# Optimization experiments

Hardware: AMD Instinct MI355X
Metric: run time of the kernel (lower is better)

The kernel has to match this reference:

```python
import jax, jax.numpy as jnp
import numpy as np

T, B = 110, 256            # max_seq_len, num dialogues (all length T)
N = T * B                  # total graph nodes
DM = 300                   # fused input dim (100 text + 100 audio + 100 visual)
F = 200                    # 2*D_e node feature dim
H = 64                     # graph_hidden_size
R = 8                      # num relations (2 speakers x 2 speakers x 2 directions)
NB = 30                    # RGCN num_bases
NC = 7                     # n_classes
DA = F + H                 # matchatt / classifier input dim
WP, WF = 10, 10            # window_past, window_future

def _build_edges():
    src, dst = [], []
    for j in range(T):
        for i in range(max(0, j - WP), min(T, j + WF + 1)):
            src.append(j); dst.append(i)
    return np.asarray(src, np.int32), np.asarray(dst, np.int32)

SRC_T, DST_T = _build_edges()                    # per-dialogue edge endpoints [E0]
DIRN = (SRC_T >= DST_T).astype(np.int32)         # direction bit: '0' iff j < i
OFF = np.arange(B, dtype=np.int32) * T
SRC = (OFF[:, None] + SRC_T[None, :]).reshape(-1)  # global src node ids, dialogue-major
DST = (OFF[:, None] + DST_T[None, :]).reshape(-1)
E = SRC.shape[0]

def _p(key, shape, scale=0.05):
    return (jax.random.normal(key, shape) * scale).astype(jnp.float32)

def setup_inputs():
    key = jax.random.key(0)
    ks = jax.random.split(key, 16)
    return {
        "textf": jax.random.normal(ks[0], (T, B, 100), jnp.float32),
        "acouf": jax.random.normal(ks[1], (T, B, 100), jnp.float32),
        "visuf": jax.random.normal(ks[2], (T, B, 100), jnp.float32),
        "speakers": jax.random.randint(ks[3], (T, B), 0, 2, jnp.int32),
        "Wf": _p(ks[4], (DM, F)), "bf": jnp.zeros((F,), jnp.float32),
        "basis": _p(ks[5], (NB, F, H)), "comp": _p(ks[6], (R, NB)),
        "root": _p(ks[7], (F, H)), "b_rgcn": jnp.zeros((H,), jnp.float32),
        "Wrel": _p(ks[8], (H, H)), "brel": jnp.zeros((H,), jnp.float32),
        "Wroot2": _p(ks[9], (H, H)),
        "Wma": _p(ks[10], (DA, DA)), "bma": jnp.zeros((DA,), jnp.float32),
        "Wl": _p(ks[11], (DA, H)), "bl": jnp.zeros((H,), jnp.float32),
        "Ws": _p(ks[12], (H, NC)), "bs": jnp.zeros((NC,), jnp.float32),
    }

def reference(textf, acouf, visuf, speakers, Wf, bf, basis, comp, root, b_rgcn,
              Wrel, brel, Wroot2, Wma, bma, Wl, bl, Ws, bs):
    src, dst = jnp.asarray(SRC), jnp.asarray(DST)
    # feature fusion: concat modalities -> linear, [T,B,300] -> [T,B,200]
    feats = jnp.concatenate([textf, acouf, visuf], axis=-1) @ Wf + bf
    x = jnp.transpose(feats, (1, 0, 2)).reshape(N, F)       # node features, dialogue-major
    # edge types from speaker ids: key '{s0}{s1}{dir}' -> s0*4 + s1*2 + dir
    s0 = speakers[SRC_T]                                    # [E0, B]
    s1 = speakers[DST_T]
    et = (s0 * 4 + s1 * 2 + jnp.asarray(DIRN)[:, None]).T.reshape(-1)  # [E]
    # --- RGCNConv (basis decomposition, per-relation mean aggregation) ---
    Wrels = jnp.einsum('rb,bfh->rfh', comp, basis)          # [R,F,H]
    xr = jnp.einsum('nf,rfh->nrh', x, Wrels)                # [N,R,H] projected per relation
    msg = xr[src, et]                                       # [E,H] gather
    seg = dst * R + et
    summ = jax.ops.segment_sum(msg, seg, num_segments=N * R).reshape(N, R, H)
    cnt = jax.ops.segment_sum(jnp.ones((E,), jnp.float32), seg, num_segments=N * R).reshape(N, R, 1)
    h1 = (summ / jnp.maximum(cnt, 1.0)).sum(1) + x @ root + b_rgcn   # [N,H]
    # --- GraphConv (sum aggregation) ---
    agg = jax.ops.segment_sum(h1[src], dst, num_segments=N)
    h2 = agg @ Wrel + brel + h1 @ Wroot2                    # [N,H]
    emotions = jnp.concatenate([x, h2], axis=-1)            # [N,DA]
    # --- nodal MatchingAttention ('general2') over full equal-length dialogues ---
    M = emotions.reshape(B, T, DA).transpose(1, 0, 2)       # [T,B,DA]
    umask = jnp.ones((B, T), jnp.float32)
    Xq = M @ Wma + bma                                      # [T,B,DA] transformed queries
    scores = jnp.einsum('tbd,sbd->tbs', Xq, M * umask.T[:, :, None])
    scores = jnp.tanh(scores * umask[None])
    alpha = jax.nn.softmax(scores, axis=-1) * umask[None]
    alpha = alpha / alpha.sum(-1, keepdims=True)
    att = jnp.einsum('tbs,sbd->tbd', alpha, M)              # [T,B,DA]
    hidden = jax.nn.relu(att @ Wl + bl)                     # dropout = identity (eval)
    logits = hidden @ Ws + bs
    logp = jax.nn.log_softmax(logits, axis=-1)              # [T,B,NC]
    # unpad/concat per dialogue (all lengths == T) -> [B*T, NC]
    return jnp.transpose(logp, (1, 0, 2)).reshape(N, NC)
```

## Files before the change

kernel.cpp:

```cpp
#include <hip/hip_runtime.h>

#define TT   110
#define BBD  256
#define NND  28160
#define WIN  10

typedef __bf16 bf16x8 __attribute__((ext_vector_type(8)));
typedef __bf16 bf16x4 __attribute__((ext_vector_type(4)));
typedef float  f32x4  __attribute__((ext_vector_type(4)));

__device__ __forceinline__ int imax(int a, int b){ return a > b ? a : b; }
__device__ __forceinline__ int imin(int a, int b){ return a < b ? a : b; }


__global__ __launch_bounds__(256) void wrels_k(
    const float* __restrict__ basis, const float* __restrict__ comp,
    const float* __restrict__ root, float* __restrict__ wrels)
{
  int idx = blockIdx.x * 256 + threadIdx.x;
  if (idx >= 115200) return;
  int r = idx / 12800, fh = idx % 12800;
  float v;
  if (r < 8) {
    v = 0.f;
    #pragma unroll
    for (int nb = 0; nb < 30; ++nb) v += comp[r*30 + nb] * basis[nb*12800 + fh];
  } else {
    v = root[fh];
  }
  wrels[idx] = v;
}

__global__ __launch_bounds__(256) void prep_k(
    const float* __restrict__ textf, const float* __restrict__ acouf,
    const float* __restrict__ visuf, const float* __restrict__ wrels,
    const float* __restrict__ Wf, const float* __restrict__ Wma,
    const float* __restrict__ Wl, const float* __restrict__ Wrel,
    const float* __restrict__ Wroot2, __bf16* __restrict__ Ain,
    __bf16* __restrict__ img)
{
  constexpr int T0 = 1126400;
  constexpr int T1 = T0 + 10240;
  constexpr int T2 = T1 + 18432;
  constexpr int T3 = T2 + 12800;
  constexpr int T4 = T3 + 2560;
  constexpr int T5 = T4 + 1024;
  for (int c = blockIdx.x * 256 + threadIdx.x; c < T5; c += gridDim.x * 256) {
    bf16x8 v;
    __bf16* dst;
    if (c < T0) {
      const int m = c / 40, cc = c - m * 40;
      const int col0 = cc << 3;
      const size_t ab = (size_t)m * 100;
      #pragma unroll
      for (int e = 0; e < 8; ++e) {
        const int col = col0 + e;
        float x = (col < 100) ? textf[ab + col]
                : (col < 200) ? acouf[ab + col - 100]
                : (col < 300) ? visuf[ab + col - 200] : 0.f;
        v[e] = (__bf16)x;
      }
      dst = Ain + (size_t)m * 320 + col0;
    } else if (c < T1) {
      const int r = c - T0;
      const int cb = r / 2560, r2 = r - cb * 2560;
      const int col = r2 / 40, ch = r2 - col * 40;
      const int cs = (ch & ~7) | ((ch ^ col) & 7);
      const int gc = (cb << 6) + col;
      #pragma unroll
      for (int e = 0; e < 8; ++e) {
        const int k = (cs << 3) + e;
        v[e] = (__bf16)((k < 300 && gc < 200) ? Wf[k*200 + gc] : 0.f);
      }
      dst = img + cb * 20480 + col * 320 + (ch << 3);
    } else if (c < T2) {
      const int r = c - T1;
      const int cb = r / 2048, r2 = r - cb * 2048;
      const int col = r2 / 32, ch = r2 - col * 32;
      const int cs = (ch & ~7) | ((ch ^ col) & 7);
      #pragma unroll
      for (int e = 0; e < 8; ++e) {
        const int k = (cs << 3) + e;
        v[e] = (__bf16)((k < 200) ? wrels[cb*12800 + k*64 + col] : 0.f);
      }
      dst = img + 81920 + cb * 16384 + col * 256 + (ch << 3);
    } else if (c < T3) {
      const int r = c - T2;
      const int cb = r / 2560, r2 = r - cb * 2560;
      const int col = r2 / 40, ch = r2 - col * 40;
      const int cs = (ch & ~7) | ((ch ^ col) & 7);
      const int gc = (cb << 6) + col;
      #pragma unroll
      for (int e = 0; e < 8; ++e) {
        const int k = (cs << 3) + e;
        v[e] = (__bf16)((k < 264 && gc < 264) ? Wma[k*264 + gc] : 0.f);
      }
      dst = img + 229376 + cb * 20480 + col * 320 + (ch << 3);
    } else if (c < T4) {
      const int r = c - T3;
      const int col = r / 40, ch = r - col * 40;
      const int cs = (ch & ~7) | ((ch ^ col) & 7);
      #pragma unroll
      for (int e = 0; e < 8; ++e) {
        const int k = (cs << 3) + e;
        v[e] = (__bf16)((k < 264) ? Wl[k*64 + col] : 0.f);
      }
      dst = img + 331776 + col * 320 + (ch << 3);
    } else {
      const int r = c - T4;
      const int col = r / 16, ch = r - col * 16;
      const int cs = (ch & ~7) | ((ch ^ col) & 7);
      #pragma unroll
      for (int e = 0; e < 8; ++e) {
        const int k = (cs << 3) + e;
        v[e] = (__bf16)((k < 64) ? Wrel[k*64 + col] : Wroot2[(k-64)*64 + col]);
      }
      dst = img + 352256 + col * 128 + (ch << 3);
    }
    *(bf16x8*)dst = v;
  }
}

template<int MODE, int NK, int KSP, int NCB, int OUT>
__global__ __launch_bounds__(256) void bgemm_k(
    const __bf16* __restrict__ A0, const __bf16* __restrict__ A1,
    const __bf16* __restrict__ Bimg, const float* __restrict__ bias,
    void* __restrict__ Cv, int Ncols)
{
  __shared__ __align__(16) __bf16 Bsh[64][KSP];
  const int tid = threadIdx.x;
  constexpr int NWT = 440 * NCB;
  constexpr int q = NWT >> 3;
  const int bid = blockIdx.x;
  const int w = (bid & 7) * q + (bid >> 3);
  const int m0 = (w / NCB) << 6;
  const int cb = w % NCB;
  const int n0 = cb << 6;

  {
    const bf16x8* src = (const bf16x8*)(Bimg + (size_t)cb * (64 * KSP));
    bf16x8* dst = (bf16x8*)&Bsh[0][0];
    constexpr int NIT = (64 * KSP / 8) / 256;
    #pragma unroll
    for (int c = 0; c < NIT; ++c) dst[c * 256 + tid] = src[c * 256 + tid];
  }
  __syncthreads();

  const int wid = tid >> 6, lane = tid & 63;
  const int wm = wid >> 1, wn = wid & 1;
  const int fr = lane & 15;
  const int fk = (lane >> 4) << 3;
  const int row0 = (lane >> 4) << 2;

  f32x4 acc[2][2];
  #pragma unroll
  for (int f = 0; f < 2; ++f)
    #pragma unroll
    for (int g = 0; g < 2; ++g) acc[f][g] = (f32x4){0.f,0.f,0.f,0.f};

  #pragma unroll
  for (int kt = 0; kt < NK; ++kt) {
    const int ko = (kt << 5) + fk;
    bf16x8 af[2];
    #pragma unroll
    for (int f = 0; f < 2; ++f) {
      const int ra = m0 + wm*32 + f*16 + fr;
      if constexpr (MODE == 2) {
        af[f] = (ko < 200) ? *(const bf16x8*)(A0 + (size_t)ra*200 + ko)
                           : *(const bf16x8*)(A1 + (size_t)ra*64 + (ko - 200));
      } else {
        constexpr int SA = (MODE == 0) ? 320 : 200;
        af[f] = *(const bf16x8*)(A0 + (size_t)ra*SA + ko);
      }
    }
    bf16x8 bfv[2];
    #pragma unroll
    for (int g = 0; g < 2; ++g) {
      const int rb_ = wn*32 + g*16 + fr;
      bfv[g] = *(const bf16x8*)&Bsh[rb_][(((ko >> 3) ^ (rb_ & 7)) << 3)];
    }
    #pragma unroll
    for (int f = 0; f < 2; ++f)
      #pragma unroll
      for (int g = 0; g < 2; ++g)
        acc[f][g] = __builtin_amdgcn_mfma_f32_16x16x32_bf16(af[f], bfv[g], acc[f][g], 0, 0, 0);
  }

  #pragma unroll
  for (int g = 0; g < 2; ++g) {
    const int col = n0 + wn*32 + g*16 + fr;
    if (col < Ncols) {
      const float bv = bias ? bias[col] : 0.f;
      #pragma unroll
      for (int f = 0; f < 2; ++f) {
        const int gm0 = m0 + wm*32 + f*16 + row0;
        #pragma unroll
        for (int r2 = 0; r2 < 4; ++r2) {
          const float v = acc[f][g][r2] + bv;
          const int gm = gm0 + r2;
          if constexpr (OUT == 1) {
            ((__bf16*)Cv)[(size_t)gm * Ncols + col] = (__bf16)v;
          } else {
            __bf16* Cb = (__bf16*)Cv;
            const size_t o = (size_t)gm * 288 + col;
            const __bf16 hi = (__bf16)v;
            Cb[o] = hi;
            Cb[(size_t)288 * NND + o] = (__bf16)(v - (float)hi);
          }
        }
      }
    }
  }
}

__global__ __launch_bounds__(512) void dialog_k(
    const __bf16* __restrict__ xr, const int* __restrict__ spk,
    const float* __restrict__ brg, const __bf16* __restrict__ Wgcimg,
    const float* __restrict__ brel, __bf16* __restrict__ h2)
{
  __shared__ __align__(16) __bf16 Xsh[75][320];
  __shared__ float  h1f[65][68];
  __shared__ __align__(16) __bf16 aggbf[56][72];
  __shared__ int ssp[TT];
  __shared__ int pc[TT + 1];
  const int bid = blockIdx.x;
  const int b = bid >> 1, half = bid & 1;
  const int t0   = half ? 55 : 0;
  const int H1LO = half ? 45 : 0;
  const int XLO  = half ? 35 : 0;
  const int tid = threadIdx.x;
  if (tid < TT) ssp[tid] = spk[tid * BBD + b];
  __syncthreads();
  if (tid < 64) {
    int v = (tid < TT) ? ssp[tid] : 0;
    #pragma unroll
    for (int o = 1; o < 64; o <<= 1) { const int u = __shfl_up(v, o); if (tid >= o) v += u; }
    pc[tid + 1] = v;
    const int tot = __shfl(v, 63);
    int v2 = (tid + 64 < TT) ? ssp[tid + 64] : 0;
    #pragma unroll
    for (int o = 1; o < 64; o <<= 1) { const int u = __shfl_up(v2, o); if (tid >= o) v2 += u; }
    if (tid + 64 < TT) pc[tid + 65] = tot + v2;
    if (tid == 0) pc[0] = 0;
  }
  for (int i = tid << 3; i < 75 * 320; i += 512 << 3) {
    const int xl = i / 320, off = i - xl * 320;
    const int j = XLO + xl;
    const size_t base = ((size_t)j * BBD + b) * 576;
    const int col = (off < 256) ? ((ssp[j] << 8) + off) : (256 + off);
    *(bf16x8*)&Xsh[xl][off] = *(const bf16x8*)&xr[base + col];
  }
  __syncthreads();
  const int w8 = tid >> 6, lane = tid & 63;
  const float bias = brg[lane];
  for (int lh = w8; lh < 65; lh += 8) {
    const int t = H1LO + lh;
    const int si2 = ssp[t] << 1;
    const int jlo = imax(t - WIN, 0), jhi = imin(t + WIN, TT - 1);
    const int n1d0 = pc[t] - pc[jlo];
    const int n0d0 = (t - jlo) - n1d0;
    const int n1d1 = pc[jhi + 1] - pc[t];
    const int n0d1 = (jhi - t + 1) - n1d1;
    const float r00 = 1.f / (float)imax(n0d0, 1);
    const float r10 = 1.f / (float)imax(n1d0, 1);
    const float r01 = 1.f / (float)imax(n0d1, 1);
    const float r11 = 1.f / (float)imax(n1d1, 1);
    float a = 0.f;
    if (t >= WIN && t < TT - WIN) {
      #pragma unroll
      for (int dj = -WIN; dj <= WIN; ++dj) {
        const int j = t + dj;
        const float v = (float)Xsh[j - XLO][((si2 + ((dj >= 0) ? 1 : 0)) << 6) + lane];
        const float w = (dj >= 0) ? (ssp[j] ? r11 : r01) : (ssp[j] ? r10 : r00);
        a = fmaf(w, v, a);
      }
    } else {
      #pragma unroll
      for (int dj = -WIN; dj <= WIN; ++dj) {
        const int j = t + dj;
        const int jc = imin(imax(j, XLO), XLO + 74);
        const float v = (float)Xsh[jc - XLO][((si2 + ((dj >= 0) ? 1 : 0)) << 6) + lane];
        float w = (dj >= 0) ? (ssp[jc] ? r11 : r01) : (ssp[jc] ? r10 : r00);
        if (j < 0 || j >= TT) w = 0.f;
        a = fmaf(w, v, a);
      }
    }
    a += (float)Xsh[t - XLO][256 + lane] + bias;
    h1f[lh][lane] = a;
  }
  __syncthreads();
  for (int lt = w8; lt < 55; lt += 8) {
    const int t = t0 + lt;
    float a = 0.f;
    if (t >= WIN && t < TT - WIN) {
      #pragma unroll
      for (int dj = -WIN; dj <= WIN; ++dj)
        a += h1f[t + dj - H1LO][lane];
    } else {
      #pragma unroll
      for (int dj = -WIN; dj <= WIN; ++dj) {
        const int j = t + dj;
        const int jc = imin(imax(j, H1LO), H1LO + 64);
        const float m = ((j >= 0) && (j < TT)) ? 1.f : 0.f;
        a = fmaf(m, h1f[jc - H1LO][lane], a);
      }
    }
    aggbf[lt][lane] = (__bf16)a;
  }
  __syncthreads();
  if (w8 < 4) {
    const int wm = w8 >> 1, wn = w8 & 1;
    const int fr = lane & 15, fk = (lane >> 4) << 3, row0 = (lane >> 4) << 2;
    const int lhh = t0 - H1LO;
    f32x4 acc[2][2];
    #pragma unroll
    for (int f = 0; f < 2; ++f)
      #pragma unroll
      for (int g = 0; g < 2; ++g) acc[f][g] = (f32x4){0.f,0.f,0.f,0.f};
    #pragma unroll
    for (int kt = 0; kt < 4; ++kt) {
      const int ko = (kt << 5) + fk;
      bf16x8 af[2];
      #pragma unroll
      for (int f = 0; f < 2; ++f) {
        const int tr = wm*32 + f*16 + fr;
        if (tr < 55) {
          if (ko < 64) {
            af[f] = *(const bf16x8*)&aggbf[tr][ko];
          } else {
            const float* src = &h1f[tr + lhh][ko - 64];
            const float4 u0 = ((const float4*)src)[0];
            const float4 u1 = ((const float4*)src)[1];
            af[f] = (bf16x8){(__bf16)u0.x,(__bf16)u0.y,(__bf16)u0.z,(__bf16)u0.w,
                             (__bf16)u1.x,(__bf16)u1.y,(__bf16)u1.z,(__bf16)u1.w};
          }
        } else af[f] = (bf16x8){0,0,0,0,0,0,0,0};
      }
      bf16x8 bfv[2];
      #pragma unroll
      for (int g = 0; g < 2; ++g) {
        const int rb_ = wn*32 + g*16 + fr;
        bfv[g] = *(const bf16x8*)(Wgcimg + rb_*128 + (((ko >> 3) ^ (rb_ & 7)) << 3));
      }
      #pragma unroll
      for (int f = 0; f < 2; ++f)
        #pragma unroll
        for (int g = 0; g < 2; ++g)
          acc[f][g] = __builtin_amdgcn_mfma_f32_16x16x32_bf16(af[f], bfv[g], acc[f][g], 0, 0, 0);
    }
    #pragma unroll
    for (int g = 0; g < 2; ++g) {
      const int col = wn*32 + g*16 + fr;
      const float bv = brel[col];
      #pragma unroll
      for (int f = 0; f < 2; ++f) {
        const int tr0 = wm*32 + f*16 + row0;
        #pragma unroll
        for (int r2 = 0; r2 < 4; ++r2) {
          const int tr = tr0 + r2;
          if (tr < 55) {
            const int t = t0 + tr;
            h2[((size_t)t * BBD + b) * 64 + col] = (__bf16)(acc[f][g][r2] + bv);
          }
        }
      }
    }
  }
}

__global__ __launch_bounds__(448) void attn_mfma_k(
    const __bf16* __restrict__ x, const __bf16* __restrict__ h2,
    const __bf16* __restrict__ Xq, __bf16* __restrict__ att)
{
  __shared__ __align__(16) __bf16 Msh [TT ][272];
  __shared__ __align__(16) __bf16 MTsh[264][136];
  __shared__ __align__(16) __bf16 Ash [112][136];
  const int b = blockIdx.x;
  const int tid = threadIdx.x;

  for (int idx = tid; idx < TT * 66; idx += 448) {
    const int s = idx / 66, c4 = idx % 66;
    const size_t node = (size_t)s * BBD + b;
    bf16x4 pk;
    if (c4 < 50) pk = *(const bf16x4*)&x [node * 200 + (c4 << 2)];
    else         pk = *(const bf16x4*)&h2[node * 64 + ((c4 - 50) << 2)];
    *(bf16x4*)&Msh[s][c4 << 2] = pk;
    const int d = c4 << 2;
    MTsh[d+0][s] = pk[0]; MTsh[d+1][s] = pk[1];
    MTsh[d+2][s] = pk[2]; MTsh[d+3][s] = pk[3];
  }
  for (int idx = tid; idx < 264 * 26; idx += 448) MTsh[idx / 26][110 + idx % 26] = (__bf16)0.f;
  for (int idx = tid; idx < 112 * 24; idx += 448) Ash[idx / 24][112 + idx % 24] = (__bf16)0.f;
  __syncthreads();

  const int wid = tid >> 6, lane = tid & 63;
  const int t0 = wid << 4;
  const int fr = lane & 15;
  const int g  = lane >> 4;
  const int fk = g << 3;

  f32x4 sacc[7];
  #pragma unroll
  for (int st = 0; st < 7; ++st) sacc[st] = (f32x4){0.f,0.f,0.f,0.f};
  const int trow = t0 + fr;
  const size_t arow = ((size_t)(trow < TT ? trow : TT - 1) * BBD + b) * 288;
  const __bf16* XqLo = Xq + (size_t)288 * NND;
  for (int kst = 0; kst < 9; ++kst) {
    const int k0 = kst << 5;
    bf16x8 aqh = *(const bf16x8*)&Xq  [arow + k0 + fk];
    bf16x8 aql = *(const bf16x8*)&XqLo[arow + k0 + fk];
    if (kst == 8 && fk != 0) {
      aqh = (bf16x8){0,0,0,0,0,0,0,0};
      aql = (bf16x8){0,0,0,0,0,0,0,0};
    }
    #pragma unroll
    for (int st = 0; st < 7; ++st) {
      bf16x8 bq;
      if (kst < 8) bq = *(const bf16x8*)&Msh[st*16 + fr][k0 + fk];
      else bq = (fk == 0) ? *(const bf16x8*)&Msh[st*16 + fr][256]
                          : (bf16x8){0,0,0,0,0,0,0,0};
      sacc[st] = __builtin_amdgcn_mfma_f32_16x16x32_bf16(aqh, bq, sacc[st], 0, 0, 0);
      sacc[st] = __builtin_amdgcn_mfma_f32_16x16x32_bf16(aql, bq, sacc[st], 0, 0, 0);
    }
  }

  #pragma unroll
  for (int r = 0; r < 4; ++r) {
    float tv[7];
    #pragma unroll
    for (int st = 0; st < 7; ++st) {
      const float e2 = __expf(2.f * sacc[st][r]);
      tv[st] = 1.f - 2.f / (e2 + 1.f);
    }
    if (fr >= 14) tv[6] = -3.0e38f;
    float mx = fmaxf(fmaxf(fmaxf(tv[0],tv[1]), fmaxf(tv[2],tv[3])),
                     fmaxf(fmaxf(tv[4],tv[5]), tv[6]));
    #pragma unroll
    for (int o = 8; o >= 1; o >>= 1) mx = fmaxf(mx, __shfl_xor(mx, o, 16));
    float e[7], sum = 0.f;
    #pragma unroll
    for (int st = 0; st < 7; ++st) { e[st] = __expf(tv[st] - mx); sum += e[st]; }
    #pragma unroll
    for (int o = 8; o >= 1; o >>= 1) sum += __shfl_xor(sum, o, 16);
    const float inv = 1.f / sum;
    const int tr = t0 + (g << 2) + r;
    #pragma unroll
    for (int st = 0; st < 7; ++st) Ash[tr][st*16 + fr] = (__bf16)(e[st] * inv);
  }
  __syncthreads();

  const int tr2 = t0 + (g << 2);
  for (int dt = 0; dt < 17; ++dt) {
    const int d0 = dt << 4;
    f32x4 pacc = (f32x4){0.f,0.f,0.f,0.f};
    #pragma unroll
    for (int kst = 0; kst < 4; ++kst) {
      const int k0 = kst << 5;
      const bf16x8 pa = *(const bf16x8*)&Ash [t0 + fr][k0 + fk];
      const bf16x8 pb = *(const bf16x8*)&MTsh[d0 + fr][k0 + fk];
      pacc = __builtin_amdgcn_mfma_f32_16x16x32_bf16(pa, pb, pacc, 0, 0, 0);
    }
    const int col = d0 + fr;
    if (col < 264) {
      #pragma unroll
      for (int r = 0; r < 4; ++r) {
        const int t = tr2 + r;
        if (t < TT) att[((size_t)t * BBD + b) * 264 + col] = (__bf16)pacc[r];
      }
    }
  }
}

__global__ __launch_bounds__(256) void final_k(
    const __bf16* __restrict__ att, const __bf16* __restrict__ Wlimg,
    const float* __restrict__ bl, const float* __restrict__ Wsm,
    const float* __restrict__ bsm, float* __restrict__ out)
{
  constexpr int KSP = 320;
  __shared__ __align__(16) __bf16 Bsh[64][KSP];
  __shared__ float hidf[64][68];
  __shared__ float Wssh[64][8];
  const int tid = threadIdx.x;
  const int bid = blockIdx.x;
  const int m0 = ((bid & 7) * 55 + (bid >> 3)) << 6;
  {
    const bf16x8* src = (const bf16x8*)Wlimg;
    bf16x8* dst = (bf16x8*)&Bsh[0][0];
    #pragma unroll
    for (int c = 0; c < 10; ++c) dst[c * 256 + tid] = src[c * 256 + tid];
    for (int i = tid; i < 512; i += 256) {
      const int k = i >> 3, cc = i & 7;
      Wssh[k][cc] = (cc < 7) ? Wsm[k*7 + cc] : 0.f;
    }
  }
  __syncthreads();
  const int wid = tid >> 6, lane = tid & 63;
  const int wm = wid >> 1, wn = wid & 1;
  const int fr = lane & 15, fk = (lane >> 4) << 3, row0 = (lane >> 4) << 2;
  f32x4 acc[2][2];
  #pragma unroll
  for (int f = 0; f < 2; ++f)
    #pragma unroll
    for (int g = 0; g < 2; ++g) acc[f][g] = (f32x4){0.f,0.f,0.f,0.f};
  #pragma unroll
  for (int kt = 0; kt < 9; ++kt) {
    const int ko = (kt << 5) + fk;
    bf16x8 af[2];
    #pragma unroll
    for (int f = 0; f < 2; ++f) {
      const int ra = m0 + wm*32 + f*16 + fr;
      af[f] = (ko < 264) ? *(const bf16x8*)(att + (size_t)ra*264 + ko)
                         : (bf16x8){0,0,0,0,0,0,0,0};
    }
    bf16x8 bfv[2];
    #pragma unroll
    for (int g = 0; g < 2; ++g) {
      const int rb_ = wn*32 + g*16 + fr;
      bfv[g] = *(const bf16x8*)&Bsh[rb_][(((ko >> 3) ^ (rb_ & 7)) << 3)];
    }
    #pragma unroll
    for (int f = 0; f < 2; ++f)
      #pragma unroll
      for (int g = 0; g < 2; ++g)
        acc[f][g] = __builtin_amdgcn_mfma_f32_16x16x32_bf16(af[f], bfv[g], acc[f][g], 0, 0, 0);
  }
  #pragma unroll
  for (int g = 0; g < 2; ++g) {
    const int col = wn*32 + g*16 + fr;
    const float bv = bl[col];
    #pragma unroll
    for (int f = 0; f < 2; ++f) {
      const int lr0 = wm*32 + f*16 + row0;
      #pragma unroll
      for (int r2 = 0; r2 < 4; ++r2)
        hidf[lr0 + r2][col] = fmaxf(acc[f][g][r2] + bv, 0.f);
    }
  }
  __syncthreads();
  const int c = tid & 7;
  const float bc = (c < 7) ? bsm[c] : 0.f;
  #pragma unroll
  for (int p = 0; p < 2; ++p) {
    const int lr = (p << 5) + (tid >> 3);
    float lg = -3.0e38f;
    if (c < 7) {
      lg = bc;
      #pragma unroll
      for (int k = 0; k < 64; ++k) lg += hidf[lr][k] * Wssh[k][c];
    }
    float mx = lg;
    #pragma unroll
    for (int o = 4; o >= 1; o >>= 1) mx = fmaxf(mx, __shfl_xor(mx, o, 8));
    float e = (c < 7) ? __expf(lg - mx) : 0.f;
    float sm = e;
    #pragma unroll
    for (int o = 4; o >= 1; o >>= 1) sm += __shfl_xor(sm, o, 8);
    if (c < 7) {
      const int gm = m0 + lr;
      const int t = gm >> 8, bb = gm & 255;
      out[((size_t)bb * TT + t) * 7 + c] = lg - mx - __logf(sm);
    }
  }
}

extern "C" void kernel_launch(void* const* d_in, const int* in_sizes, int n_in,
                              void* d_out, int out_size, void* d_ws, size_t ws_size,
                              hipStream_t stream)
{
  const float* textf  = (const float*)d_in[0];
  const float* acouf  = (const float*)d_in[1];
  const float* visuf  = (const float*)d_in[2];
  const int*   spk    = (const int*)  d_in[3];
  const float* Wf     = (const float*)d_in[4];
  const float* bfv    = (const float*)d_in[5];
  const float* basis  = (const float*)d_in[6];
  const float* comp   = (const float*)d_in[7];
  const float* root   = (const float*)d_in[8];
  const float* brg    = (const float*)d_in[9];
  const float* Wrel   = (const float*)d_in[10];
  const float* brel   = (const float*)d_in[11];
  const float* Wroot2 = (const float*)d_in[12];
  const float* Wma    = (const float*)d_in[13];
  const float* bma    = (const float*)d_in[14];
  const float* Wl     = (const float*)d_in[15];
  const float* bl     = (const float*)d_in[16];
  const float* Wsm    = (const float*)d_in[17];
  const float* bsm    = (const float*)d_in[18];

  float* ws = (float*)d_ws;
  float*  wrels = ws;
  __bf16* img   = (__bf16*)(ws + 115200);
  __bf16* Ain   = (__bf16*)(ws + 295424);
  __bf16* xb    = (__bf16*)(ws + 4801024);
  __bf16* xr    = (__bf16*)(ws + 7617024);
  __bf16* h2    = (__bf16*)(ws + 15727104);
  __bf16* Xqb   = (__bf16*)(ws + 16628224);
  __bf16* attb  = xr;
  float*  outp  = (float*)d_out;

  __bf16* Wfimg  = img;
  __bf16* wrimg  = img + 81920;
  __bf16* Wmaimg = img + 229376;
  __bf16* Wlimg  = img + 331776;
  __bf16* Wgcimg = img + 352256;

  wrels_k<<<450, 256, 0, stream>>>(basis, comp, root, wrels);
  prep_k<<<2048, 256, 0, stream>>>(textf, acouf, visuf, wrels, Wf, Wma, Wl,
                                   Wrel, Wroot2, Ain, img);
  bgemm_k<0,10,320,4,1><<<1760, 256, 0, stream>>>(Ain, nullptr, Wfimg, bfv, xb, 200);
  bgemm_k<1,7,256,9,1><<<3960, 256, 0, stream>>>(xb, nullptr, wrimg, nullptr, xr, 576);
  dialog_k<<<512, 512, 0, stream>>>(xr, spk, brg, Wgcimg, brel, h2);
  bgemm_k<2,9,320,5,2><<<2200, 256, 0, stream>>>(xb, h2, Wmaimg, bma, Xqb, 264);
  attn_mfma_k<<<256, 448, 0, stream>>>(xb, h2, Xqb, attb);
  final_k<<<440, 256, 0, stream>>>(attb, Wlimg, bl, Wsm, bsm, outp);
}
```

Measured before the change: 153.7 us.

## Fuse final classifier into attention kernel and skip unused relation-GEMM stores

The final projection (Wl GEMM, ReLU, Ws logits, log-softmax) moves into the attention kernel. The attention output stays in shared memory (reusing Msh) instead of being written to global memory and read back by a separate launch. The relation GEMM epilogue also writes only the column blocks matching each source node's speaker (plus the root block), which cuts global store traffic. In exchange, the fused tail runs on only 256 blocks with Wl read straight from global memory, and it relies on downstream code reading only the speaker-matching columns.

```diff
diff --git a/kernel.cpp b/kernel.cpp
--- a/kernel.cpp
+++ b/kernel.cpp
@@ -125,7 +125,7 @@
 __global__ __launch_bounds__(256) void bgemm_k(
     const __bf16* __restrict__ A0, const __bf16* __restrict__ A1,
     const __bf16* __restrict__ Bimg, const float* __restrict__ bias,
-    void* __restrict__ Cv, int Ncols)
+    void* __restrict__ Cv, int Ncols, const int* __restrict__ spkm)
 {
   __shared__ __align__(16) __bf16 Bsh[64][KSP];
   const int tid = threadIdx.x;
@@ -187,25 +187,34 @@
   }
 
   #pragma unroll
-  for (int g = 0; g < 2; ++g) {
-    const int col = n0 + wn*32 + g*16 + fr;
-    if (col < Ncols) {
-      const float bv = bias ? bias[col] : 0.f;
-      #pragma unroll
-      for (int f = 0; f < 2; ++f) {
-        const int gm0 = m0 + wm*32 + f*16 + row0;
+  for (int f = 0; f < 2; ++f) {
+    const int gm0 = m0 + wm*32 + f*16 + row0;
+    int sp[4];
+    if constexpr (MODE == 1) {
+      #pragma unroll
+      for (int r2 = 0; r2 < 4; ++r2) sp[r2] = spkm[gm0 + r2];
+    }
+    #pragma unroll
+    for (int g = 0; g < 2; ++g) {
+      const int col = n0 + wn*32 + g*16 + fr;
+      if (col < Ncols) {
+        const float bv = bias ? bias[col] : 0.f;
         #pragma unroll
         for (int r2 = 0; r2 < 4; ++r2) {
           const float v = acc[f][g][r2] + bv;
           const int gm = gm0 + r2;
-          if constexpr (OUT == 1) {
-            ((__bf16*)Cv)[(size_t)gm * Ncols + col] = (__bf16)v;
-          } else {
-            __bf16* Cb = (__bf16*)Cv;
-            const size_t o = (size_t)gm * 288 + col;
-            const __bf16 hi = (__bf16)v;
-            Cb[o] = hi;
-            Cb[(size_t)288 * NND + o] = (__bf16)(v - (float)hi);
+          bool dow = true;
+          if constexpr (MODE == 1) dow = (cb == 8) || ((cb >> 2) == sp[r2]);
+          if (dow) {
+            if constexpr (OUT == 1) {
+              ((__bf16*)Cv)[(size_t)gm * Ncols + col] = (__bf16)v;
+            } else {
+              __bf16* Cb = (__bf16*)Cv;
+              const size_t o = (size_t)gm * 288 + col;
+              const __bf16 hi = (__bf16)v;
+              Cb[o] = hi;
+              Cb[(size_t)288 * NND + o] = (__bf16)(v - (float)hi);
+            }
           }
         }
       }
@@ -368,9 +377,11 @@
   }
 }
 
-__global__ __launch_bounds__(448) void attn_mfma_k(
+__global__ __launch_bounds__(448) void attn_fused_k(
     const __bf16* __restrict__ x, const __bf16* __restrict__ h2,
-    const __bf16* __restrict__ Xq, __bf16* __restrict__ att)
+    const __bf16* __restrict__ Xq, const __bf16* __restrict__ Wlimg,
+    const float* __restrict__ bl, const float* __restrict__ Wsm,
+    const float* __restrict__ bsm, float* __restrict__ out)
 {
   __shared__ __align__(16) __bf16 Msh [TT ][272];
   __shared__ __align__(16) __bf16 MTsh[264][136];
@@ -398,6 +409,7 @@
   const int fr = lane & 15;
   const int g  = lane >> 4;
   const int fk = g << 3;
+  const int row0 = g << 2;
 
   f32x4 sacc[7];
   #pragma unroll
@@ -449,6 +461,7 @@
   }
   __syncthreads();
 
+  __bf16 (*attsh)[272] = Msh;
   const int tr2 = t0 + (g << 2);
   for (int dt = 0; dt < 17; ++dt) {
     const int d0 = dt << 4;
@@ -465,100 +478,68 @@
       #pragma unroll
       for (int r = 0; r < 4; ++r) {
         const int t = tr2 + r;
-        if (t < TT) att[((size_t)t * BBD + b) * 264 + col] = (__bf16)pacc[r];
-      }
-    }
-  }
-}
-
-__global__ __launch_bounds__(256) void final_k(
-    const __bf16* __restrict__ att, const __bf16* __restrict__ Wlimg,
-    const float* __restrict__ bl, const float* __restrict__ Wsm,
-    const float* __restrict__ bsm, float* __restrict__ out)
-{
-  constexpr int KSP = 320;
-  __shared__ __align__(16) __bf16 Bsh[64][KSP];
-  __shared__ float hidf[64][68];
-  __shared__ float Wssh[64][8];
-  const int tid = threadIdx.x;
-  const int bid = blockIdx.x;
-  const int m0 = ((bid & 7) * 55 + (bid >> 3)) << 6;
-  {
-    const bf16x8* src = (const bf16x8*)Wlimg;
-    bf16x8* dst = (bf16x8*)&Bsh[0][0];
-    #pragma unroll
-    for (int c = 0; c < 10; ++c) dst[c * 256 + tid] = src[c * 256 + tid];
-    for (int i = tid; i < 512; i += 256) {
-      const int k = i >> 3, cc = i & 7;
-      Wssh[k][cc] = (cc < 7) ? Wsm[k*7 + cc] : 0.f;
-    }
-  }
-  __syncthreads();
-  const int wid = tid >> 6, lane = tid & 63;
-  const int wm = wid >> 1, wn = wid & 1;
-  const int fr = lane & 15, fk = (lane >> 4) << 3, row0 = (lane >> 4) << 2;
-  f32x4 acc[2][2];
-  #pragma unroll
-  for (int f = 0; f < 2; ++f)
-    #pragma unroll
-    for (int g = 0; g < 2; ++g) acc[f][g] = (f32x4){0.f,0.f,0.f,0.f};
-  #pragma unroll
-  for (int kt = 0; kt < 9; ++kt) {
-    const int ko = (kt << 5) + fk;
-    bf16x8 af[2];
-    #pragma unroll
-    for (int f = 0; f < 2; ++f) {
-      const int ra = m0 + wm*32 + f*16 + fr;
-      af[f] = (ko < 264) ? *(const bf16x8*)(att + (size_t)ra*264 + ko)
-                         : (bf16x8){0,0,0,0,0,0,0,0};
-    }
-    bf16x8 bfv[2];
-    #pragma unroll
-    for (int g = 0; g < 2; ++g) {
-      const int rb_ = wn*32 + g*16 + fr;
-      bfv[g] = *(const bf16x8*)&Bsh[rb_][(((ko >> 3) ^ (rb_ & 7)) << 3)];
-    }
-    #pragma unroll
-    for (int f = 0; f < 2; ++f)
-      #pragma unroll
-      for (int g = 0; g < 2; ++g)
-        acc[f][g] = __builtin_amdgcn_mfma_f32_16x16x32_bf16(af[f], bfv[g], acc[f][g], 0, 0, 0);
-  }
-  #pragma unroll
-  for (int g = 0; g < 2; ++g) {
-    const int col = wn*32 + g*16 + fr;
+        if (t < TT) attsh[t][col] = (__bf16)pacc[r];
+      }
+    }
+  }
+  __syncthreads();
+
+  float* Wssh = (float*)&MTsh[0][0];
+  for (int i = tid; i < 512; i += 448) {
+    const int k = i >> 3, cc = i & 7;
+    Wssh[(k << 3) + cc] = (cc < 7) ? Wsm[k*7 + cc] : 0.f;
+  }
+
+  float (*hidf)[68] = (float(*)[68])&Ash[0][0];
+  f32x4 hacc[4];
+  #pragma unroll
+  for (int gg = 0; gg < 4; ++gg) hacc[gg] = (f32x4){0.f,0.f,0.f,0.f};
+  #pragma unroll
+  for (int kst = 0; kst < 9; ++kst) {
+    const int ko = (kst << 5) + fk;
+    const int ar = t0 + fr;
+    bf16x8 af;
+    if (ko < 264 && ar < TT) af = *(const bf16x8*)&attsh[ar][ko];
+    else af = (bf16x8){0,0,0,0,0,0,0,0};
+    #pragma unroll
+    for (int gg = 0; gg < 4; ++gg) {
+      const int rb_ = gg*16 + fr;
+      const bf16x8 bfv = *(const bf16x8*)(Wlimg + rb_*320 + (((ko >> 3) ^ (rb_ & 7)) << 3));
+      hacc[gg] = __builtin_amdgcn_mfma_f32_16x16x32_bf16(af, bfv, hacc[gg], 0, 0, 0);
+    }
+  }
+  #pragma unroll
+  for (int gg = 0; gg < 4; ++gg) {
+    const int col = gg*16 + fr;
     const float bv = bl[col];
     #pragma unroll
-    for (int f = 0; f < 2; ++f) {
-      const int lr0 = wm*32 + f*16 + row0;
-      #pragma unroll
-      for (int r2 = 0; r2 < 4; ++r2)
-        hidf[lr0 + r2][col] = fmaxf(acc[f][g][r2] + bv, 0.f);
-    }
-  }
-  __syncthreads();
+    for (int r = 0; r < 4; ++r) {
+      const int row = t0 + row0 + r;
+      if (row < TT) hidf[row][col] = fmaxf(hacc[gg][r] + bv, 0.f);
+    }
+  }
+  __syncthreads();
+
   const int c = tid & 7;
   const float bc = (c < 7) ? bsm[c] : 0.f;
   #pragma unroll
   for (int p = 0; p < 2; ++p) {
-    const int lr = (p << 5) + (tid >> 3);
-    float lg = -3.0e38f;
-    if (c < 7) {
-      lg = bc;
-      #pragma unroll
-      for (int k = 0; k < 64; ++k) lg += hidf[lr][k] * Wssh[k][c];
-    }
-    float mx = lg;
-    #pragma unroll
-    for (int o = 4; o >= 1; o >>= 1) mx = fmaxf(mx, __shfl_xor(mx, o, 8));
-    float e = (c < 7) ? __expf(lg - mx) : 0.f;
-    float sm = e;
-    #pragma unroll
-    for (int o = 4; o >= 1; o >>= 1) sm += __shfl_xor(sm, o, 8);
-    if (c < 7) {
-      const int gm = m0 + lr;
-      const int t = gm >> 8, bb = gm & 255;
-      out[((size_t)bb * TT + t) * 7 + c] = lg - mx - __logf(sm);
+    const int lr = p * 56 + (tid >> 3);
+    if (lr < TT) {
+      float lg = -3.0e38f;
+      if (c < 7) {
+        lg = bc;
+        #pragma unroll
+        for (int k = 0; k < 64; ++k) lg += hidf[lr][k] * Wssh[(k << 3) + c];
+      }
+      float mx = lg;
+      #pragma unroll
+      for (int o = 4; o >= 1; o >>= 1) mx = fmaxf(mx, __shfl_xor(mx, o, 8));
+      float e = (c < 7) ? __expf(lg - mx) : 0.f;
+      float sm = e;
+      #pragma unroll
+      for (int o = 4; o >= 1; o >>= 1) sm += __shfl_xor(sm, o, 8);
+      if (c < 7) out[((size_t)b * TT + lr) * 7 + c] = lg - mx - __logf(sm);
     }
   }
 }
@@ -595,7 +576,6 @@
   __bf16* xr    = (__bf16*)(ws + 7617024);
   __bf16* h2    = (__bf16*)(ws + 15727104);
   __bf16* Xqb   = (__bf16*)(ws + 16628224);
-  __bf16* attb  = xr;
   float*  outp  = (float*)d_out;
 
   __bf16* Wfimg  = img;
@@ -607,10 +587,9 @@
   wrels_k<<<450, 256, 0, stream>>>(basis, comp, root, wrels);
   prep_k<<<2048, 256, 0, stream>>>(textf, acouf, visuf, wrels, Wf, Wma, Wl,
                                    Wrel, Wroot2, Ain, img);
-  bgemm_k<0,10,320,4,1><<<1760, 256, 0, stream>>>(Ain, nullptr, Wfimg, bfv, xb, 200);
-  bgemm_k<1,7,256,9,1><<<3960, 256, 0, stream>>>(xb, nullptr, wrimg, nullptr, xr, 576);
+  bgemm_k<0,10,320,4,1><<<1760, 256, 0, stream>>>(Ain, nullptr, Wfimg, bfv, xb, 200, nullptr);
+  bgemm_k<1,7,256,9,1><<<3960, 256, 0, stream>>>(xb, nullptr, wrimg, nullptr, xr, 576, spk);
   dialog_k<<<512, 512, 0, stream>>>(xr, spk, brg, Wgcimg, brel, h2);
-  bgemm_k<2,9,320,5,2><<<2200, 256, 0, stream>>>(xb, h2, Wmaimg, bma, Xqb, 264);
-  attn_mfma_k<<<256, 448, 0, stream>>>(xb, h2, Xqb, attb);
-  final_k<<<440, 256, 0, stream>>>(attb, Wlimg, bl, Wsm, bsm, outp);
+  bgemm_k<2,9,320,5,2><<<2200, 256, 0, stream>>>(xb, h2, Wmaimg, bma, Xqb, 264, nullptr);
+  attn_fused_k<<<256, 448, 0, stream>>>(xb, h2, Xqb, Wlimg, bl, Wsm, bsm, outp);
 }
```

Result: no change. 151.7 us (-1.3%).
